# Kernel tuning notes

Measured on AMD Instinct MI355X. Metric: run time of the kernel, lower is better.

## Reference

```python
import jax, jax.numpy as jnp
import numpy as np

GAMMA = 9.6
BETA = 0.83
LAMDA = 10.0
EPS = 1e-12

B, D, C = 1024, 512, 10000


def _l2norm(x):
    # torch F.normalize: x / max(||x||_2, eps)
    n = jnp.sqrt(jnp.sum(x * x, axis=1, keepdims=True))
    return x / jnp.maximum(n, EPS)


def setup_inputs() -> dict:
    key = jax.random.key(0)
    k1, k2, k3, k4 = jax.random.split(key, 4)
    inp = jax.random.normal(k1, (B, D), dtype=jnp.float32)
    # xavier-uniform-like init for the classifier weight
    limit = float(np.sqrt(6.0 / (C + D)))
    weight = jax.random.uniform(k2, (C, D), dtype=jnp.float32, minval=-limit, maxval=limit)
    class_weight = jax.random.uniform(k3, (C,), dtype=jnp.float32)  # per-class margins in [0,1)
    label = jax.random.randint(k4, (B,), 0, C, dtype=jnp.int32)
    return {"input": inp, "weight": weight, "class_weight": class_weight, "label": label}


def reference(input, weight, class_weight, label):
    x = _l2norm(input)            # [B, D]
    w = _l2norm(weight)           # [C, D]
    fea = x @ w.T                 # [B, C] cosine logits

    # sp_i = fea[i, label_i]; logit_{ij} = sn_ij - sp_i + beta * m_j  (j != label_i)
    sp = jnp.take_along_axis(fea, label[:, None], axis=1)           # [B, 1]
    logits = GAMMA * (fea - sp + BETA * class_weight[None, :])      # [B, C]
    pos_mask = label[:, None] == jnp.arange(C, dtype=label.dtype)[None, :]
    logits = jnp.where(pos_mask, -jnp.inf, logits)                  # drop positive column
    lse = jax.scipy.special.logsumexp(logits, axis=1)               # [B]
    loss = jax.nn.softplus(lse)                                     # [B]

    # inter-class similarity penalty
    score = jnp.clip(w @ w.T, -1.0, 1.0)                            # [C, C]
    score = score * (1.0 - jnp.eye(C, dtype=score.dtype))           # zero diagonal
    s = jnp.max(score[label], axis=1)                               # [B]
    loss_w = jax.nn.softplus(jnp.mean(s) + 0.5)

    loss = loss + LAMDA * loss_w
    return fea, jnp.mean(loss)
```

## Files before the change

### kernel.cpp

```cpp
#include <hip/hip_runtime.h>
#include <math.h>

#define GAMMA 9.6f
#define BETA  0.83f
#define LAMDA 10.0f
#define B_ 1024
#define D_ 512
#define C_ 10000
#define M0_ 20.0f

#define WS_XB   0
#define WS_WB   1048576
#define WS_SU   11288576
#define WS_T    11292672
#define WS_SP   11296768

typedef __attribute__((ext_vector_type(8))) short short8;
typedef __attribute__((ext_vector_type(4))) float floatx4;

__device__ __forceinline__ unsigned enc_f(float f) {
    unsigned i = __float_as_uint(f);
    return (i & 0x80000000u) ? ~i : (i | 0x80000000u);
}
__device__ __forceinline__ float dec_f(unsigned u) {
    return (u & 0x80000000u) ? __uint_as_float(u ^ 0x80000000u)
                             : __uint_as_float(~u);
}
__device__ __forceinline__ float softplus_f(float x) {
    return (x > 30.f) ? x : log1pf(expf(x));
}
__device__ __forceinline__ unsigned short f2bf_rne(float f) {
    unsigned u = __float_as_uint(f);
    u += 0x7FFFu + ((u >> 16) & 1u);
    return (unsigned short)(u >> 16);
}

__global__ __launch_bounds__(128) void normcvt_kernel(
    const float* __restrict__ input, const float* __restrict__ weight,
    unsigned short* __restrict__ xb, unsigned short* __restrict__ wb,
    unsigned* __restrict__ s_u, float* __restrict__ T) {
    int row = blockIdx.x;
    int tid = threadIdx.x;
    if (row < B_ && tid == 0) { s_u[row] = 0u; T[row] = 0.f; }

    const float* src = (row < B_) ? (input + (size_t)row * D_)
                                  : (weight + (size_t)(row - B_) * D_);
    float4 v = *(const float4*)(src + tid * 4);
    float ss = v.x * v.x + v.y * v.y + v.z * v.z + v.w * v.w;
    #pragma unroll
    for (int o = 32; o > 0; o >>= 1) ss += __shfl_xor(ss, o, 64);
    __shared__ float red[2];
    if ((tid & 63) == 0) red[tid >> 6] = ss;
    __syncthreads();
    float inv = 1.0f / fmaxf(sqrtf(red[0] + red[1]), 1e-12f);
    unsigned short* dst = (row < B_) ? (xb + (size_t)row * D_)
                                     : (wb + (size_t)(row - B_) * D_);
    ushort4 o4;
    o4.x = f2bf_rne(v.x * inv);
    o4.y = f2bf_rne(v.y * inv);
    o4.z = f2bf_rne(v.z * inv);
    o4.w = f2bf_rne(v.w * inv);
    *(ushort4*)(dst + tid * 4) = o4;
}

#define BM 128
#define BN 128
#define BK 32
#define NSTEP (D_ / BK)
#define NTILE_M 16
#define NTILE_N 79
#define NWG (NTILE_M * NTILE_N)

__global__ __launch_bounds__(256) void mfma_gemm_kernel(
    const unsigned short* __restrict__ xb, const unsigned short* __restrict__ wb,
    const int* __restrict__ label, const float* __restrict__ cw,
    float* __restrict__ fea, unsigned* __restrict__ s_u,
    float* __restrict__ T, float* __restrict__ sp) {
    __shared__ __align__(16) unsigned short As[2][BM * BK];
    __shared__ __align__(16) unsigned short Bs[2][BM * BK];

    const int tid = threadIdx.x;
    const int orig = (blockIdx.x & 7) * (NWG / 8) + (blockIdx.x >> 3);
    const int m0 = (orig & 15) * BM;
    const int n0 = (orig >> 4) * BN;
    const bool feaTile = (m0 < B_);

    const int arow = tid >> 2;
    const int kc8 = (tid & 3) * 8;
    const unsigned short* asrc[2];
    const unsigned short* bsrc[2];
    #pragma unroll
    for (int q = 0; q < 2; q++) {
        int rm = m0 + arow + q * 64;
        const unsigned short* ab;
        if (rm < B_) ab = xb + (size_t)rm * D_;
        else         ab = wb + (size_t)label[rm - B_] * D_;
        asrc[q] = ab + kc8;
        int rn = n0 + arow + q * 64;
        if (rn >= C_) rn = C_ - 1;
        bsrc[q] = wb + (size_t)rn * D_ + kc8;
    }

    const int lane = tid & 63;
    const int wv = tid >> 6;
    const int wr = (wv >> 1) * 64;
    const int wc = (wv & 1) * 64;
    const int l15 = lane & 15;
    const int hi = lane >> 4;

    floatx4 acc[4][4];
    #pragma unroll
    for (int i = 0; i < 4; i++)
        #pragma unroll
        for (int j = 0; j < 4; j++)
            acc[i][j] = (floatx4){0.f, 0.f, 0.f, 0.f};

#define STAGE(buf, kt)                                                         \
    {                                                                          \
        _Pragma("unroll")                                                      \
        for (int q = 0; q < 2; q++) {                                          \
            __builtin_amdgcn_global_load_lds(                                  \
                (const __attribute__((address_space(1))) void*)(asrc[q] + (kt)),\
                (__attribute__((address_space(3))) void*)((char*)&As[buf][0] + tid * 16 + q * 4096), \
                16, 0, 0);                                                     \
            __builtin_amdgcn_global_load_lds(                                  \
                (const __attribute__((address_space(1))) void*)(bsrc[q] + (kt)),\
                (__attribute__((address_space(3))) void*)((char*)&Bs[buf][0] + tid * 16 + q * 4096), \
                16, 0, 0);                                                     \
        }                                                                      \
    }

    STAGE(0, 0);
    __syncthreads();

    int cur = 0;
    for (int t = 0; t < NSTEP; ++t) {
        int ktn = (t + 1) * BK;
        if (ktn < D_) STAGE(cur ^ 1, ktn);
        short8 a[4], b[4];
        #pragma unroll
        for (int i = 0; i < 4; i++)
            a[i] = *(const short8*)&As[cur][(wr + i * 16 + l15) * BK + hi * 8];
        #pragma unroll
        for (int j = 0; j < 4; j++)
            b[j] = *(const short8*)&Bs[cur][(wc + j * 16 + l15) * BK + hi * 8];
        #pragma unroll
        for (int i = 0; i < 4; i++)
            #pragma unroll
            for (int j = 0; j < 4; j++)
                acc[i][j] = __builtin_amdgcn_mfma_f32_16x16x32_bf16(
                    a[i], b[j], acc[i][j], 0, 0, 0);
        __syncthreads();
        cur ^= 1;
    }

    if (feaTile) {
        int lbl_ir[4][4];
        #pragma unroll
        for (int i = 0; i < 4; i++)
            #pragma unroll
            for (int r = 0; r < 4; r++)
                lbl_ir[i][r] = label[m0 + wr + i * 16 + hi * 4 + r];
        float cwj[4];
        #pragma unroll
        for (int j = 0; j < 4; j++) {
            int n = n0 + wc + j * 16 + l15;
            cwj[j] = (n < C_) ? cw[n] : 0.f;
        }
        float rs[4][4];
        #pragma unroll
        for (int i = 0; i < 4; i++)
            #pragma unroll
            for (int r = 0; r < 4; r++) rs[i][r] = 0.f;

        #pragma unroll
        for (int i = 0; i < 4; i++) {
            #pragma unroll
            for (int j = 0; j < 4; j++) {
                int n = n0 + wc + j * 16 + l15;
                if (n < C_) {
                    int m = m0 + wr + i * 16 + hi * 4;
                    float* dst = fea + (size_t)m * C_ + n;
                    #pragma unroll
                    for (int r = 0; r < 4; r++) {
                        float v = acc[i][j][r];
                        dst[(size_t)r * C_] = v;
                        int l = lbl_ir[i][r];
                        if (n == l) sp[m + r] = v;
                        else rs[i][r] += expf(GAMMA * (v + BETA * cwj[j]) - M0_);
                    }
                }
            }
        }
        #pragma unroll
        for (int i = 0; i < 4; i++) {
            #pragma unroll
            for (int r = 0; r < 4; r++) {
                float s = rs[i][r];
                #pragma unroll
                for (int o = 8; o > 0; o >>= 1) s += __shfl_xor(s, o, 64);
                if (l15 == 0)
                    atomicAdd(T + (m0 + wr + i * 16 + hi * 4 + r), s);
            }
        }
    } else {
        #pragma unroll
        for (int i = 0; i < 4; i++) {
            #pragma unroll
            for (int r = 0; r < 4; r++) {
                int row = m0 - B_ + wr + i * 16 + hi * 4 + r;
                int l = label[row];
                float vmax = -2.f;
                #pragma unroll
                for (int j = 0; j < 4; j++) {
                    int n = n0 + wc + j * 16 + l15;
                    float v = fminf(fmaxf(acc[i][j][r], -1.f), 1.f);
                    if (n == l) v = 0.f;
                    if (n < C_) vmax = fmaxf(vmax, v);
                }
                #pragma unroll
                for (int o = 8; o > 0; o >>= 1)
                    vmax = fmaxf(vmax, __shfl_xor(vmax, o, 64));
                if (l15 == 0) atomicMax(s_u + row, enc_f(vmax));
            }
        }
    }
}

__global__ __launch_bounds__(1024) void final_kernel(
    const unsigned* __restrict__ s_u, const float* __restrict__ T,
    const float* __restrict__ sp, float* __restrict__ out_loss) {
    int tid = threadIdx.x;
    float lse = M0_ + logf(T[tid]) - GAMMA * sp[tid];
    float lr = softplus_f(lse);
    float sv = dec_f(s_u[tid]);
    #pragma unroll
    for (int o = 32; o > 0; o >>= 1) {
        lr += __shfl_xor(lr, o, 64);
        sv += __shfl_xor(sv, o, 64);
    }
    __shared__ float red_l[16], red_s[16];
    if ((tid & 63) == 0) { red_l[tid >> 6] = lr; red_s[tid >> 6] = sv; }
    __syncthreads();
    if (tid == 0) {
        float tl = 0.f, ts = 0.f;
        #pragma unroll
        for (int w = 0; w < 16; w++) { tl += red_l[w]; ts += red_s[w]; }
        float loss_w = softplus_f(ts / (float)B_ + 0.5f);
        *out_loss = tl / (float)B_ + LAMDA * loss_w;
    }
}

extern "C" void kernel_launch(void* const* d_in, const int* in_sizes, int n_in,
                              void* d_out, int out_size, void* d_ws, size_t ws_size,
                              hipStream_t stream) {
    const float* input  = (const float*)d_in[0];
    const float* weight = (const float*)d_in[1];
    const float* cw     = (const float*)d_in[2];
    const int*   label  = (const int*)d_in[3];
    float* out = (float*)d_out;

    char* ws = (char*)d_ws;
    unsigned short* xb = (unsigned short*)(ws + WS_XB);
    unsigned short* wb = (unsigned short*)(ws + WS_WB);
    unsigned* s_u      = (unsigned*)(ws + WS_SU);
    float*    T        = (float*)(ws + WS_T);
    float*    sp       = (float*)(ws + WS_SP);

    normcvt_kernel<<<B_ + C_, 128, 0, stream>>>(input, weight, xb, wb, s_u, T);

    mfma_gemm_kernel<<<NWG, 256, 0, stream>>>(xb, wb, label, cw, out, s_u, T, sp);

    final_kernel<<<1, 1024, 0, stream>>>(s_u, T, sp, out + (size_t)B_ * C_);
}
```

Measured before the change: 70.92 us.

## Restructure GEMM main loop with split-K LDS stages, XOR swizzle, and finer waits

Doubles the K tile to 64, split into two 32-wide sub-stages per buffer, and uses explicit vmcnt waits with raw barriers so loads for the next tile overlap MFMA work at sub-stage granularity. LDS rows are XOR-swizzled on both the global-to-LDS write and the fragment read to reduce bank conflicts. MFMA sections are bracketed with s_setprio to favour matrix issue. LDS use doubles, and the hand-tuned vmcnt counts depend on exactly four outstanding loads per stage, so the scheme is fragile.

```diff
diff --git a/kernel.cpp b/kernel.cpp
--- a/kernel.cpp
+++ b/kernel.cpp
@@ -65,8 +65,8 @@
 
 #define BM 128
 #define BN 128
-#define BK 32
-#define NSTEP (D_ / BK)
+#define BK 64
+#define NKT (D_ / BK)
 #define NTILE_M 16
 #define NTILE_N 79
 #define NWG (NTILE_M * NTILE_N)
@@ -76,8 +76,8 @@
     const int* __restrict__ label, const float* __restrict__ cw,
     float* __restrict__ fea, unsigned* __restrict__ s_u,
     float* __restrict__ T, float* __restrict__ sp) {
-    __shared__ __align__(16) unsigned short As[2][BM * BK];
-    __shared__ __align__(16) unsigned short Bs[2][BM * BK];
+    __shared__ __align__(16) unsigned short As[2][2][128 * 32];
+    __shared__ __align__(16) unsigned short Bs[2][2][128 * 32];
 
     const int tid = threadIdx.x;
     const int orig = (blockIdx.x & 7) * (NWG / 8) + (blockIdx.x >> 3);
@@ -85,20 +85,20 @@
     const int n0 = (orig >> 4) * BN;
     const bool feaTile = (m0 < B_);
 
-    const int arow = tid >> 2;
-    const int kc8 = (tid & 3) * 8;
+    const int srow = tid >> 2;
+    const int kchunk = (tid & 3) ^ ((tid >> 3) & 3);
     const unsigned short* asrc[2];
     const unsigned short* bsrc[2];
     #pragma unroll
     for (int q = 0; q < 2; q++) {
-        int rm = m0 + arow + q * 64;
+        int rm = m0 + srow + q * 64;
         const unsigned short* ab;
         if (rm < B_) ab = xb + (size_t)rm * D_;
         else         ab = wb + (size_t)label[rm - B_] * D_;
-        asrc[q] = ab + kc8;
-        int rn = n0 + arow + q * 64;
+        asrc[q] = ab + kchunk * 8;
+        int rn = n0 + srow + q * 64;
         if (rn >= C_) rn = C_ - 1;
-        bsrc[q] = wb + (size_t)rn * D_ + kc8;
+        bsrc[q] = wb + (size_t)rn * D_ + kchunk * 8;
     }
 
     const int lane = tid & 63;
@@ -107,6 +107,7 @@
     const int wc = (wv & 1) * 64;
     const int l15 = lane & 15;
     const int hi = lane >> 4;
+    const int xs = (l15 >> 1) & 3;
 
     floatx4 acc[4][4];
     #pragma unroll
@@ -115,43 +116,57 @@
         for (int j = 0; j < 4; j++)
             acc[i][j] = (floatx4){0.f, 0.f, 0.f, 0.f};
 
-#define STAGE(buf, kt)                                                         \
+#define STAGE(bufn, ksn, ktelem)                                               \
     {                                                                          \
         _Pragma("unroll")                                                      \
         for (int q = 0; q < 2; q++) {                                          \
             __builtin_amdgcn_global_load_lds(                                  \
-                (const __attribute__((address_space(1))) void*)(asrc[q] + (kt)),\
-                (__attribute__((address_space(3))) void*)((char*)&As[buf][0] + tid * 16 + q * 4096), \
+                (const __attribute__((address_space(1))) void*)(asrc[q] + (ktelem)), \
+                (__attribute__((address_space(3))) void*)((char*)&As[bufn][ksn][0] + (q * 256 + tid) * 16), \
                 16, 0, 0);                                                     \
             __builtin_amdgcn_global_load_lds(                                  \
-                (const __attribute__((address_space(1))) void*)(bsrc[q] + (kt)),\
-                (__attribute__((address_space(3))) void*)((char*)&Bs[buf][0] + tid * 16 + q * 4096), \
+                (const __attribute__((address_space(1))) void*)(bsrc[q] + (ktelem)), \
+                (__attribute__((address_space(3))) void*)((char*)&Bs[bufn][ksn][0] + (q * 256 + tid) * 16), \
                 16, 0, 0);                                                     \
         }                                                                      \
     }
 
-    STAGE(0, 0);
-    __syncthreads();
-
-    int cur = 0;
-    for (int t = 0; t < NSTEP; ++t) {
-        int ktn = (t + 1) * BK;
-        if (ktn < D_) STAGE(cur ^ 1, ktn);
-        short8 a[4], b[4];
-        #pragma unroll
-        for (int i = 0; i < 4; i++)
-            a[i] = *(const short8*)&As[cur][(wr + i * 16 + l15) * BK + hi * 8];
-        #pragma unroll
-        for (int j = 0; j < 4; j++)
-            b[j] = *(const short8*)&Bs[cur][(wc + j * 16 + l15) * BK + hi * 8];
-        #pragma unroll
-        for (int i = 0; i < 4; i++)
+    STAGE(0, 0, 0);
+    STAGE(0, 1, 32);
+
+    #pragma unroll
+    for (int t = 0; t < NKT; ++t) {
+        const int cur = t & 1;
+        #pragma unroll
+        for (int ks = 0; ks < 2; ++ks) {
+            if (t == NKT - 1 && ks == 1)
+                asm volatile("s_waitcnt vmcnt(0)" ::: "memory");
+            else
+                asm volatile("s_waitcnt vmcnt(4)" ::: "memory");
+            __builtin_amdgcn_s_barrier();
+            __builtin_amdgcn_sched_barrier(0);
+
+            short8 a[4], b[4];
+            #pragma unroll
+            for (int i = 0; i < 4; i++)
+                a[i] = *(const short8*)&As[cur][ks]
+                        [(wr + i * 16 + l15) * 32 + ((hi ^ xs) << 3)];
             #pragma unroll
             for (int j = 0; j < 4; j++)
-                acc[i][j] = __builtin_amdgcn_mfma_f32_16x16x32_bf16(
-                    a[i], b[j], acc[i][j], 0, 0, 0);
-        __syncthreads();
-        cur ^= 1;
+                b[j] = *(const short8*)&Bs[cur][ks]
+                        [(wc + j * 16 + l15) * 32 + ((hi ^ xs) << 3)];
+
+            if (t + 1 < NKT) STAGE(cur ^ 1, ks, (t + 1) * 64 + ks * 32);
+
+            __builtin_amdgcn_s_setprio(1);
+            #pragma unroll
+            for (int i = 0; i < 4; i++)
+                #pragma unroll
+                for (int j = 0; j < 4; j++)
+                    acc[i][j] = __builtin_amdgcn_mfma_f32_16x16x32_bf16(
+                        a[i], b[j], acc[i][j], 0, 0, 0);
+            __builtin_amdgcn_s_setprio(0);
+        }
     }
 
     if (feaTile) {
```

Measured after the change: 75.48 us. 6.4% more time.

## Enlarge GEMM M-tile to 256 and XOR-swizzle LDS layout

Applied to the files above, without the earlier changes.

Doubles the M tile from 128 to 256 rows, so each wave computes a 128x64 block with 8x4 MFMA accumulators. This halves the number of workgroups and raises reuse of each loaded B tile. It also XOR-swizzles the k-chunk placement in LDS to cut bank conflicts on the short8 fragment reads. The epilogue is restructured per i-block to keep register pressure down. In exchange, the accumulators double and LDS grows, which may lower occupancy, and fewer workgroups (632) could leave the 256 CUs less evenly loaded.

```diff
diff --git a/kernel.cpp b/kernel.cpp
--- a/kernel.cpp
+++ b/kernel.cpp
@@ -63,11 +63,11 @@
     *(ushort4*)(dst + tid * 4) = o4;
 }
 
-#define BM 128
+#define BM 256
 #define BN 128
 #define BK 32
 #define NSTEP (D_ / BK)
-#define NTILE_M 16
+#define NTILE_M 8
 #define NTILE_N 79
 #define NWG (NTILE_M * NTILE_N)
 
@@ -76,41 +76,43 @@
     const int* __restrict__ label, const float* __restrict__ cw,
     float* __restrict__ fea, unsigned* __restrict__ s_u,
     float* __restrict__ T, float* __restrict__ sp) {
-    __shared__ __align__(16) unsigned short As[2][BM * BK];
-    __shared__ __align__(16) unsigned short Bs[2][BM * BK];
+    __shared__ __align__(16) unsigned short As[2][256 * 32];
+    __shared__ __align__(16) unsigned short Bs[2][128 * 32];
 
     const int tid = threadIdx.x;
     const int orig = (blockIdx.x & 7) * (NWG / 8) + (blockIdx.x >> 3);
-    const int m0 = (orig & 15) * BM;
-    const int n0 = (orig >> 4) * BN;
+    const int m0 = (orig & 7) * BM;
+    const int n0 = (orig >> 3) * BN;
     const bool feaTile = (m0 < B_);
 
-    const int arow = tid >> 2;
-    const int kc8 = (tid & 3) * 8;
-    const unsigned short* asrc[2];
+    const int srow = tid >> 2;
+    const int kchunk = (tid & 3) ^ ((tid >> 3) & 3);
+    const unsigned short* asrc[4];
+    #pragma unroll
+    for (int q = 0; q < 4; q++) {
+        int rm = m0 + q * 64 + srow;
+        if (rm < B_) asrc[q] = xb + (size_t)rm * D_ + kchunk * 8;
+        else         asrc[q] = wb + (size_t)label[rm - B_] * D_ + kchunk * 8;
+    }
     const unsigned short* bsrc[2];
     #pragma unroll
     for (int q = 0; q < 2; q++) {
-        int rm = m0 + arow + q * 64;
-        const unsigned short* ab;
-        if (rm < B_) ab = xb + (size_t)rm * D_;
-        else         ab = wb + (size_t)label[rm - B_] * D_;
-        asrc[q] = ab + kc8;
-        int rn = n0 + arow + q * 64;
+        int rn = n0 + q * 64 + srow;
         if (rn >= C_) rn = C_ - 1;
-        bsrc[q] = wb + (size_t)rn * D_ + kc8;
+        bsrc[q] = wb + (size_t)rn * D_ + kchunk * 8;
     }
 
     const int lane = tid & 63;
     const int wv = tid >> 6;
-    const int wr = (wv >> 1) * 64;
+    const int wm = (wv >> 1) * 128;
     const int wc = (wv & 1) * 64;
     const int l15 = lane & 15;
     const int hi = lane >> 4;
-
-    floatx4 acc[4][4];
-    #pragma unroll
-    for (int i = 0; i < 4; i++)
+    const int xs = (l15 >> 1) & 3;
+
+    floatx4 acc[8][4];
+    #pragma unroll
+    for (int i = 0; i < 8; i++)
         #pragma unroll
         for (int j = 0; j < 4; j++)
             acc[i][j] = (floatx4){0.f, 0.f, 0.f, 0.f};
@@ -118,16 +120,17 @@
 #define STAGE(buf, kt)                                                         \
     {                                                                          \
         _Pragma("unroll")                                                      \
-        for (int q = 0; q < 2; q++) {                                          \
+        for (int q = 0; q < 4; q++)                                            \
             __builtin_amdgcn_global_load_lds(                                  \
                 (const __attribute__((address_space(1))) void*)(asrc[q] + (kt)),\
-                (__attribute__((address_space(3))) void*)((char*)&As[buf][0] + tid * 16 + q * 4096), \
+                (__attribute__((address_space(3))) void*)((char*)&As[buf][0] + (q * 256 + tid) * 16), \
                 16, 0, 0);                                                     \
+        _Pragma("unroll")                                                      \
+        for (int q = 0; q < 2; q++)                                            \
             __builtin_amdgcn_global_load_lds(                                  \
                 (const __attribute__((address_space(1))) void*)(bsrc[q] + (kt)),\
-                (__attribute__((address_space(3))) void*)((char*)&Bs[buf][0] + tid * 16 + q * 4096), \
+                (__attribute__((address_space(3))) void*)((char*)&Bs[buf][0] + (q * 256 + tid) * 16), \
                 16, 0, 0);                                                     \
-        }                                                                      \
     }
 
     STAGE(0, 0);
@@ -137,15 +140,15 @@
     for (int t = 0; t < NSTEP; ++t) {
         int ktn = (t + 1) * BK;
         if (ktn < D_) STAGE(cur ^ 1, ktn);
-        short8 a[4], b[4];
-        #pragma unroll
-        for (int i = 0; i < 4; i++)
-            a[i] = *(const short8*)&As[cur][(wr + i * 16 + l15) * BK + hi * 8];
+        short8 a[8], b[4];
+        #pragma unroll
+        for (int i = 0; i < 8; i++)
+            a[i] = *(const short8*)&As[cur][((wm + i * 16 + l15) << 5) + ((hi ^ xs) << 3)];
         #pragma unroll
         for (int j = 0; j < 4; j++)
-            b[j] = *(const short8*)&Bs[cur][(wc + j * 16 + l15) * BK + hi * 8];
-        #pragma unroll
-        for (int i = 0; i < 4; i++)
+            b[j] = *(const short8*)&Bs[cur][((wc + j * 16 + l15) << 5) + ((hi ^ xs) << 3)];
+        #pragma unroll
+        for (int i = 0; i < 8; i++)
             #pragma unroll
             for (int j = 0; j < 4; j++)
                 acc[i][j] = __builtin_amdgcn_mfma_f32_16x16x32_bf16(
@@ -155,61 +158,48 @@
     }
 
     if (feaTile) {
-        int lbl_ir[4][4];
-        #pragma unroll
-        for (int i = 0; i < 4; i++)
-            #pragma unroll
-            for (int r = 0; r < 4; r++)
-                lbl_ir[i][r] = label[m0 + wr + i * 16 + hi * 4 + r];
         float cwj[4];
         #pragma unroll
         for (int j = 0; j < 4; j++) {
             int n = n0 + wc + j * 16 + l15;
             cwj[j] = (n < C_) ? cw[n] : 0.f;
         }
-        float rs[4][4];
-        #pragma unroll
-        for (int i = 0; i < 4; i++)
-            #pragma unroll
-            for (int r = 0; r < 4; r++) rs[i][r] = 0.f;
-
-        #pragma unroll
-        for (int i = 0; i < 4; i++) {
+        #pragma unroll
+        for (int i = 0; i < 8; i++) {
+            int mbase = m0 + wm + i * 16 + hi * 4;
+            int lblr[4];
+            #pragma unroll
+            for (int r = 0; r < 4; r++) lblr[r] = label[mbase + r];
+            float rsr[4] = {0.f, 0.f, 0.f, 0.f};
             #pragma unroll
             for (int j = 0; j < 4; j++) {
                 int n = n0 + wc + j * 16 + l15;
                 if (n < C_) {
-                    int m = m0 + wr + i * 16 + hi * 4;
-                    float* dst = fea + (size_t)m * C_ + n;
+                    float* dst = fea + (size_t)mbase * C_ + n;
                     #pragma unroll
                     for (int r = 0; r < 4; r++) {
                         float v = acc[i][j][r];
                         dst[(size_t)r * C_] = v;
-                        int l = lbl_ir[i][r];
-                        if (n == l) sp[m + r] = v;
-                        else rs[i][r] += expf(GAMMA * (v + BETA * cwj[j]) - M0_);
+                        if (n == lblr[r]) sp[mbase + r] = v;
+                        else rsr[r] += expf(GAMMA * (v + BETA * cwj[j]) - M0_);
                     }
                 }
             }
-        }
-        #pragma unroll
-        for (int i = 0; i < 4; i++) {
             #pragma unroll
             for (int r = 0; r < 4; r++) {
-                float s = rs[i][r];
+                float s = rsr[r];
                 #pragma unroll
                 for (int o = 8; o > 0; o >>= 1) s += __shfl_xor(s, o, 64);
-                if (l15 == 0)
-                    atomicAdd(T + (m0 + wr + i * 16 + hi * 4 + r), s);
+                if (l15 == 0) atomicAdd(T + mbase + r, s);
             }
         }
     } else {
         #pragma unroll
-        for (int i = 0; i < 4; i++) {
+        for (int i = 0; i < 8; i++) {
+            int rbase = m0 - B_ + wm + i * 16 + hi * 4;
             #pragma unroll
             for (int r = 0; r < 4; r++) {
-                int row = m0 - B_ + wr + i * 16 + hi * 4 + r;
-                int l = label[row];
+                int l = label[rbase + r];
                 float vmax = -2.f;
                 #pragma unroll
                 for (int j = 0; j < 4; j++) {
@@ -221,7 +211,7 @@
                 #pragma unroll
                 for (int o = 8; o > 0; o >>= 1)
                     vmax = fmaxf(vmax, __shfl_xor(vmax, o, 64));
-                if (l15 == 0) atomicMax(s_u + row, enc_f(vmax));
+                if (l15 == 0) atomicMax(s_u + rbase + r, enc_f(vmax));
             }
         }
     }
```

Result: slower. 130.7 us (+84.3%).
